# Kernel optimization log

Hardware: AMD Instinct MI355X
Metric: run time of the kernel (lower is better)

## Reference

```python
import jax, jax.numpy as jnp
import numpy as np

HK, WK = 7, 11  # local_k


def _local_mask(H, W):
    # Equivalent to the torch buffer: 0 inside the hk x wk window centered on the
    # query position (for odd hk, wk), -inf outside. Shape (N, N), N = H*W.
    n = jnp.arange(H * W)
    hq, wq = n // W, n % W
    dh = jnp.abs(hq[:, None] - hq[None, :])
    dw = jnp.abs(wq[:, None] - wq[None, :])
    allowed = (dh <= HK // 2) & (dw <= WK // 2)
    return jnp.where(allowed, 0.0, -jnp.inf).astype(jnp.float32)


def setup_inputs() -> dict:
    key = jax.random.key(0)
    k1, k2, k3 = jax.random.split(key, 3)
    B, H, W, C = 8, 32, 64, 512
    N = H * W
    x = jax.random.normal(k1, (B, N, C), dtype=jnp.float32)
    qkv_w = jax.random.normal(k2, (3 * C, C), dtype=jnp.float32) * (C ** -0.5)
    proj_w = jax.random.normal(k3, (C, C), dtype=jnp.float32) * (C ** -0.5)
    proj_b = jnp.zeros((C,), dtype=jnp.float32)
    return {"x": x, "qkv_w": qkv_w, "proj_w": proj_w, "proj_b": proj_b, "H": H, "W": W}


def reference(x, qkv_w, proj_w, proj_b, H, W):
    B, N, C = x.shape
    num_heads = 8
    head_dim = C // num_heads
    scale = head_dim ** -0.5

    # qkv: Linear(dim, 3*dim, bias=False) -> (B, N, 3, heads, head_dim)
    qkv = (x @ qkv_w.T).reshape(B, N, 3, num_heads, head_dim)
    q = qkv[:, :, 0].transpose(0, 2, 1, 3) * scale  # (B, h, N, d)
    k = qkv[:, :, 1].transpose(0, 2, 1, 3)
    v = qkv[:, :, 2].transpose(0, 2, 1, 3)

    attn = jnp.einsum('bhnd,bhmd->bhnm', q, k)  # (B, h, N, N)
    attn = attn + _local_mask(H, W)  # broadcast over (B, h)
    attn = jax.nn.softmax(attn, axis=-1)

    out = jnp.einsum('bhnm,bhmd->bhnd', attn, v)  # (B, h, N, d)
    out = out.transpose(0, 2, 1, 3).reshape(B, N, C)
    return out @ proj_w.T + proj_b
```

## Files before the change

### kernel.cpp

```cpp
#include <hip/hip_runtime.h>
#include <hip/hip_bf16.h>

#define B_SZ 8
#define H_SZ 32
#define W_SZ 64
#define N_SZ 2048
#define C_SZ 512
#define NH 8
#define HD 64

using u16 = unsigned short;
typedef __attribute__((ext_vector_type(8))) short s16x8;
typedef __attribute__((ext_vector_type(4))) float f32x4;

__device__ __forceinline__ float bf2f(u16 u) {
    union { unsigned int i; float f; } c; c.i = ((unsigned int)u) << 16; return c.f;
}
__device__ __forceinline__ u16 f2bf(float f) {
    union { float f; unsigned int i; } c; c.f = f;
    unsigned int r = c.i + 0x7fffu + ((c.i >> 16) & 1u);
    return (u16)(r >> 16);
}

#define GLL16(gp, lp) __builtin_amdgcn_global_load_lds( \
    (const __attribute__((address_space(1))) unsigned int*)(gp), \
    (__attribute__((address_space(3))) unsigned int*)(lp), 16, 0, 0)

__device__ __forceinline__ int lds_off(int row, int chunk) {
    return (row * 8 + (chunk ^ (row & 7))) * 8;
}

#define NX4 2097152
#define NQ4 196608
#define NP4 65536
__global__ __launch_bounds__(256)
void conv_all(const float* __restrict__ x, const float* __restrict__ qw,
              const float* __restrict__ pw, u16* __restrict__ xb,
              u16* __restrict__ qwb, u16* __restrict__ pwb)
{
    const int i = blockIdx.x * 256 + threadIdx.x;
    const float* src; u16* dst; int idx; float sc = 1.0f;
    if (i < NX4)             { src = x;  dst = xb;  idx = i; }
    else if (i < NX4 + NQ4)  { src = qw; dst = qwb; idx = i - NX4;
                               if (idx < 65536) sc = 0.125f; }
    else                     { src = pw; dst = pwb; idx = i - NX4 - NQ4; }
    const float4 v = ((const float4*)src)[idx];
    ushort4 o = { f2bf(v.x * sc), f2bf(v.y * sc), f2bf(v.z * sc), f2bf(v.w * sc) };
    ((ushort4*)dst)[idx] = o;
}

template<int MODE, int NB>
__global__ __launch_bounds__(512)
void gemm9(const u16* __restrict__ A, const u16* __restrict__ Bw,
           const float* __restrict__ bias,
           u16* __restrict__ q_ws, u16* __restrict__ k_ws, u16* __restrict__ v_ws,
           float* __restrict__ outp)
{
    __shared__ u16 As[3][256 * 64];
    __shared__ u16 Bs[3][128 * 64];
    const int t = threadIdx.x;
    const int chunk = gridDim.x >> 3;
    const int wg = (blockIdx.x & 7) * chunk + (blockIdx.x >> 3);
    const int m0 = (wg / NB) * 256;
    const int n0 = (wg % NB) * 128;
    const int wave = t >> 6, lane = t & 63;
    const int wm = (wave >> 2) * 128;
    const int wn = (wave & 3) * 32;
    const int l16 = lane & 15, quad = lane >> 4;
    const int srow = t >> 3;
    const int sch  = (t & 7) ^ (srow & 7);

    const u16* Ab = A  + (size_t)(m0 + srow) * C_SZ + sch * 8;
    const u16* Bb = Bw + (size_t)(n0 + srow) * C_SZ + sch * 8;

    f32x4 acc[8][2] = {};

#define SA(b, k0, g) GLL16(Ab + (size_t)(64 * (g)) * C_SZ + (k0), \
                           &As[b][(g) * 4096 + t * 8])
#define SB(b, k0, g) GLL16(Bb + (size_t)(64 * (g)) * C_SZ + (k0), \
                           &Bs[b][(g) * 4096 + t * 8])

    #pragma unroll
    for (int tb = 0; tb < 2; ++tb) {
        SA(tb, tb * 64, 0); SA(tb, tb * 64, 1); SA(tb, tb * 64, 2); SA(tb, tb * 64, 3);
        SB(tb, tb * 64, 0); SB(tb, tb * 64, 1);
    }
    asm volatile("s_waitcnt vmcnt(6)" ::: "memory");
    __builtin_amdgcn_s_barrier();
    __builtin_amdgcn_sched_barrier(0);

    #pragma unroll
    for (int tt = 0; tt < 8; ++tt) {
        const int ct = tt % 3;
        const int nt = (tt + 2) % 3;
        const int k2 = (tt + 2) * 64;

        s16x8 af[4][2], bf[2][2];
        #pragma unroll
        for (int i = 0; i < 4; ++i) {
            const int R = wm + 16 * i + l16;
            af[i][0] = *(const s16x8*)&As[ct][lds_off(R, quad)];
            af[i][1] = *(const s16x8*)&As[ct][lds_off(R, 4 + quad)];
        }
        #pragma unroll
        for (int j = 0; j < 2; ++j) {
            const int R = wn + 16 * j + l16;
            bf[j][0] = *(const s16x8*)&Bs[ct][lds_off(R, quad)];
            bf[j][1] = *(const s16x8*)&Bs[ct][lds_off(R, 4 + quad)];
        }
        if (tt < 6) { SA(nt, k2, 0); SA(nt, k2, 1); SB(nt, k2, 0); }
        __builtin_amdgcn_sched_barrier(0);
        __builtin_amdgcn_s_barrier();
        asm volatile("s_waitcnt lgkmcnt(0)" ::: "memory");
        __builtin_amdgcn_sched_barrier(0);
        __builtin_amdgcn_s_setprio(1);
        #pragma unroll
        for (int i = 0; i < 4; ++i)
            #pragma unroll
            for (int j = 0; j < 2; ++j) {
                acc[i][j] = __builtin_amdgcn_mfma_f32_16x16x32_bf16(af[i][0], bf[j][0], acc[i][j], 0, 0, 0);
                acc[i][j] = __builtin_amdgcn_mfma_f32_16x16x32_bf16(af[i][1], bf[j][1], acc[i][j], 0, 0, 0);
            }
        __builtin_amdgcn_s_setprio(0);
        __builtin_amdgcn_sched_barrier(0);
        __builtin_amdgcn_s_barrier();
        __builtin_amdgcn_sched_barrier(0);

        #pragma unroll
        for (int i = 0; i < 4; ++i) {
            const int R = wm + 64 + 16 * i + l16;
            af[i][0] = *(const s16x8*)&As[ct][lds_off(R, quad)];
            af[i][1] = *(const s16x8*)&As[ct][lds_off(R, 4 + quad)];
        }
        if (tt < 6) { SA(nt, k2, 2); SA(nt, k2, 3); SB(nt, k2, 1); }
        if (tt < 6)       asm volatile("s_waitcnt vmcnt(6)" ::: "memory");
        else if (tt == 6) asm volatile("s_waitcnt vmcnt(0)" ::: "memory");
        __builtin_amdgcn_sched_barrier(0);
        __builtin_amdgcn_s_barrier();
        asm volatile("s_waitcnt lgkmcnt(0)" ::: "memory");
        __builtin_amdgcn_sched_barrier(0);
        __builtin_amdgcn_s_setprio(1);
        #pragma unroll
        for (int i = 0; i < 4; ++i)
            #pragma unroll
            for (int j = 0; j < 2; ++j) {
                acc[4 + i][j] = __builtin_amdgcn_mfma_f32_16x16x32_bf16(af[i][0], bf[j][0], acc[4 + i][j], 0, 0, 0);
                acc[4 + i][j] = __builtin_amdgcn_mfma_f32_16x16x32_bf16(af[i][1], bf[j][1], acc[4 + i][j], 0, 0, 0);
            }
        __builtin_amdgcn_s_setprio(0);
        __builtin_amdgcn_sched_barrier(0);
        __builtin_amdgcn_s_barrier();
        __builtin_amdgcn_sched_barrier(0);
    }
#undef SA
#undef SB

    if (MODE == 0) {
        const int bb  = m0 >> 11;
        const int nnb = (m0 & 2047) + wm + (quad << 2);
        if (n0 >= 1024) {
            #pragma unroll
            for (int j = 0; j < 2; ++j) {
                const int c  = n0 - 1024 + wn + 16 * j + l16;
                const int h  = c >> 6, dd = c & 63;
                u16* vp = v_ws + (((size_t)bb * NH + h) * HD + dd) * N_SZ + nnb;
                #pragma unroll
                for (int i = 0; i < 8; ++i) {
                    ushort4 st = { f2bf(acc[i][j][0]), f2bf(acc[i][j][1]),
                                   f2bf(acc[i][j][2]), f2bf(acc[i][j][3]) };
                    *(ushort4*)(vp + 16 * i) = st;
                }
            }
        } else {
            u16* T = (n0 < 512) ? q_ws : k_ws;
            const int nq = n0 & 511;
            #pragma unroll
            for (int j = 0; j < 2; ++j) {
                const int gn = nq + wn + 16 * j + l16;
                const int h  = (gn >> 6) & 7, dd = gn & 63;
                u16* tp = T + (((size_t)bb * NH + h) * N_SZ + nnb) * HD + dd;
                #pragma unroll
                for (int i = 0; i < 8; ++i)
                    #pragma unroll
                    for (int r = 0; r < 4; ++r)
                        tp[(size_t)(16 * i + r) * HD] = f2bf(acc[i][j][r]);
            }
        }
    } else {
        #pragma unroll
        for (int j = 0; j < 2; ++j) {
            const int gn = n0 + wn + 16 * j + l16;
            const float bv = bias[gn];
            #pragma unroll
            for (int i = 0; i < 8; ++i)
                #pragma unroll
                for (int r = 0; r < 4; ++r)
                    outp[(size_t)(m0 + wm + 16 * i + (quad << 2) + r) * C_SZ + gn]
                        = acc[i][j][r] + bv;
        }
    }
}

__global__ __launch_bounds__(256)
void attn_mfma(const u16* __restrict__ q_ws, const u16* __restrict__ k_ws,
               const u16* __restrict__ vt_ws, u16* __restrict__ o_ws)
{
    __shared__ u16 KV[2][64 * 64];
    __shared__ u16 Ps[4][16 * 40];

    const int t = threadIdx.x, wave = t >> 6, lane = t & 63;
    const int l16 = lane & 15, quad = lane >> 4;
    const int u  = blockIdx.x;
    const int p  = u & 15;
    const int bh = u >> 4;
    const int r0 = 2 * p, r1 = 2 * p + 1;
    const size_t base = (size_t)bh * (N_SZ * HD);
    const int srow = t >> 3;
    const int sch  = (t & 7) ^ (srow & 7);

    const u16* qg = q_ws + base + (size_t)r0 * (64 * HD);
    u16* Qst = &KV[0][0];
    #pragma unroll
    for (int g = 0; g < 4; ++g)
        GLL16(qg + (size_t)(srow + 32 * g) * 64 + sch * 8, Qst + g * 2048 + t * 8);
    __syncthreads();

    s16x8 aQ[2][2];
    #pragma unroll
    for (int s = 0; s < 2; ++s) {
        const int Rq = 64 * s + 16 * wave + l16;
        aQ[s][0] = *(const s16x8*)&Qst[lds_off(Rq, quad)];
        aQ[s][1] = *(const s16x8*)&Qst[lds_off(Rq, 4 + quad)];
    }

    const int kb = min(max(16 * wave - 8, 0), 32);

    f32x4 accO[2][4] = {};
    float lp[2][4] = {};

    const int hlo = (r0 - 3 < 0) ? 0 : r0 - 3;
    const int hhi = (r1 + 3 > H_SZ - 1) ? H_SZ - 1 : r1 + 3;

    for (int hh = hlo; hh <= hhi; ++hh) {
        __syncthreads();
        const u16* kg = k_ws + base + (size_t)hh * (64 * HD);
        GLL16(kg + (size_t)srow        * 64 + sch * 8, &KV[0][t * 8]);
        GLL16(kg + (size_t)(srow + 32) * 64 + sch * 8, &KV[0][2048 + t * 8]);
        const u16* vg = vt_ws + base + (size_t)hh * 64;
        GLL16(vg + (size_t)srow        * N_SZ + sch * 8, &KV[1][t * 8]);
        GLL16(vg + (size_t)(srow + 32) * N_SZ + sch * 8, &KV[1][2048 + t * 8]);
        __syncthreads();

        s16x8 bK[2][2];
        #pragma unroll
        for (int j = 0; j < 2; ++j) {
            const int Rk = kb + 16 * j + l16;
            bK[j][0] = *(const s16x8*)&KV[0][lds_off(Rk, quad)];
            bK[j][1] = *(const s16x8*)&KV[0][lds_off(Rk, 4 + quad)];
        }
        s16x8 vf[4];
        #pragma unroll
        for (int j = 0; j < 4; ++j)
            vf[j] = *(const s16x8*)&KV[1][lds_off(16 * j + l16, (kb >> 3) + quad)];

        #pragma unroll
        for (int s = 0; s < 2; ++s) {
            const int dh = hh - (r0 + s);
            if (dh * dh > 9) continue;
            f32x4 z[2] = {{0.f,0.f,0.f,0.f},{0.f,0.f,0.f,0.f}};
            #pragma unroll
            for (int j = 0; j < 2; ++j) {
                z[j] = __builtin_amdgcn_mfma_f32_16x16x32_bf16(aQ[s][0], bK[j][0], z[j], 0, 0, 0);
                z[j] = __builtin_amdgcn_mfma_f32_16x16x32_bf16(aQ[s][1], bK[j][1], z[j], 0, 0, 0);
            }
            #pragma unroll
            for (int j = 0; j < 2; ++j) {
                const int ww = kb + 16 * j + l16;
                #pragma unroll
                for (int r = 0; r < 4; ++r) {
                    const int dw = ww - (16 * wave + quad * 4 + r);
                    const float pv = (dw * dw <= 25) ? __expf(z[j][r]) : 0.f;
                    const u16 pb = f2bf(pv);
                    lp[s][r] += bf2f(pb);
                    Ps[wave][(quad * 4 + r) * 40 + 16 * j + l16] = pb;
                }
            }
            s16x8 aP = *(const s16x8*)&Ps[wave][l16 * 40 + quad * 8];
            #pragma unroll
            for (int j = 0; j < 4; ++j)
                accO[s][j] = __builtin_amdgcn_mfma_f32_16x16x32_bf16(aP, vf[j], accO[s][j], 0, 0, 0);
        }
    }

    #pragma unroll
    for (int s = 0; s < 2; ++s)
        #pragma unroll
        for (int r = 0; r < 4; ++r) {
            lp[s][r] += __shfl_xor(lp[s][r], 1);
            lp[s][r] += __shfl_xor(lp[s][r], 2);
            lp[s][r] += __shfl_xor(lp[s][r], 4);
            lp[s][r] += __shfl_xor(lp[s][r], 8);
        }

    const int bb = bh >> 3, h = bh & 7;
    #pragma unroll
    for (int s = 0; s < 2; ++s)
        #pragma unroll
        for (int j = 0; j < 4; ++j)
            #pragma unroll
            for (int r = 0; r < 4; ++r) {
                const int row = (r0 + s) * 64 + 16 * wave + quad * 4 + r;
                o_ws[((size_t)bb * N_SZ + row) * C_SZ + h * 64 + 16 * j + l16]
                    = f2bf(accO[s][j][r] / lp[s][r]);
            }
}

extern "C" void kernel_launch(void* const* d_in, const int* in_sizes, int n_in,
                              void* d_out, int out_size, void* d_ws, size_t ws_size,
                              hipStream_t stream)
{
    const float* x      = (const float*)d_in[0];
    const float* qkv_w  = (const float*)d_in[1];
    const float* proj_w = (const float*)d_in[2];
    const float* proj_b = (const float*)d_in[3];
    float* outp = (float*)d_out;

    const size_t seg = (size_t)B_SZ * NH * N_SZ * HD;
    u16* q_ws = (u16*)d_ws;
    u16* k_ws = q_ws + seg;
    u16* v_ws = k_ws + seg;
    u16* o_ws = v_ws + seg;
    u16* xb   = o_ws + seg;
    u16* qwb  = xb + (size_t)16384 * 512;
    u16* pwb  = qwb + (size_t)1536 * 512;

    conv_all<<<9216, 256, 0, stream>>>(x, qkv_w, proj_w, xb, qwb, pwb);

    gemm9<0, 12><<<768, 512, 0, stream>>>(xb, qwb, nullptr,
                                          q_ws, k_ws, v_ws, nullptr);
    attn_mfma<<<B_SZ * NH * (H_SZ / 2), 256, 0, stream>>>(q_ws, k_ws, v_ws, o_ws);
    gemm9<1, 4><<<256, 512, 0, stream>>>(o_ws, pwb, proj_b,
                                         nullptr, nullptr, nullptr, outp);
}
```

Measured before the change: 177.0 us.

## Enlarge GEMM tile to 256x256 with double-buffered LDS pipeline

Widens each GEMM workgroup's N tile from 128 to 256, so each wave computes a 128x64 block. The LDS pipeline goes from three buffers to two, and the A and B loads for the next k-step are split across the four MFMA phases. This raises arithmetic intensity per LDS byte loaded and halves the grid size (384 and 128 blocks). The cost is more accumulator registers, possibly lower occupancy, and fewer blocks than the mi355x's 256 CUs for the projection GEMM, which may leave CUs idle.

```diff
diff --git a/kernel.cpp b/kernel.cpp
--- a/kernel.cpp
+++ b/kernel.cpp
@@ -51,21 +51,21 @@
 
 template<int MODE, int NB>
 __global__ __launch_bounds__(512)
-void gemm9(const u16* __restrict__ A, const u16* __restrict__ Bw,
-           const float* __restrict__ bias,
-           u16* __restrict__ q_ws, u16* __restrict__ k_ws, u16* __restrict__ v_ws,
-           float* __restrict__ outp)
+void gemm10(const u16* __restrict__ A, const u16* __restrict__ Bw,
+            const float* __restrict__ bias,
+            u16* __restrict__ q_ws, u16* __restrict__ k_ws, u16* __restrict__ v_ws,
+            float* __restrict__ outp)
 {
-    __shared__ u16 As[3][256 * 64];
-    __shared__ u16 Bs[3][128 * 64];
+    __shared__ u16 As[2][256 * 64];
+    __shared__ u16 Bs[2][256 * 64];
     const int t = threadIdx.x;
     const int chunk = gridDim.x >> 3;
     const int wg = (blockIdx.x & 7) * chunk + (blockIdx.x >> 3);
     const int m0 = (wg / NB) * 256;
-    const int n0 = (wg % NB) * 128;
+    const int n0 = (wg % NB) * 256;
     const int wave = t >> 6, lane = t & 63;
     const int wm = (wave >> 2) * 128;
-    const int wn = (wave & 3) * 32;
+    const int wn = (wave & 3) * 64;
     const int l16 = lane & 15, quad = lane >> 4;
     const int srow = t >> 3;
     const int sch  = (t & 7) ^ (srow & 7);
@@ -73,42 +73,40 @@
     const u16* Ab = A  + (size_t)(m0 + srow) * C_SZ + sch * 8;
     const u16* Bb = Bw + (size_t)(n0 + srow) * C_SZ + sch * 8;
 
-    f32x4 acc[8][2] = {};
-
-#define SA(b, k0, g) GLL16(Ab + (size_t)(64 * (g)) * C_SZ + (k0), \
-                           &As[b][(g) * 4096 + t * 8])
-#define SB(b, k0, g) GLL16(Bb + (size_t)(64 * (g)) * C_SZ + (k0), \
-                           &Bs[b][(g) * 4096 + t * 8])
-
-    #pragma unroll
-    for (int tb = 0; tb < 2; ++tb) {
-        SA(tb, tb * 64, 0); SA(tb, tb * 64, 1); SA(tb, tb * 64, 2); SA(tb, tb * 64, 3);
-        SB(tb, tb * 64, 0); SB(tb, tb * 64, 1);
-    }
-    asm volatile("s_waitcnt vmcnt(6)" ::: "memory");
+    f32x4 acc[8][4] = {};
+
+#define SA10(b, k0, g) GLL16(Ab + (size_t)(64 * (g)) * C_SZ + (k0), \
+                             &As[b][(g) * 4096 + t * 8])
+#define SB10(b, k0, g) GLL16(Bb + (size_t)(64 * (g)) * C_SZ + (k0), \
+                             &Bs[b][(g) * 4096 + t * 8])
+
+    SA10(0, 0, 0); SA10(0, 0, 1); SA10(0, 0, 2); SA10(0, 0, 3);
+    SB10(0, 0, 0); SB10(0, 0, 1); SB10(0, 0, 2); SB10(0, 0, 3);
+    asm volatile("s_waitcnt vmcnt(0)" ::: "memory");
     __builtin_amdgcn_s_barrier();
     __builtin_amdgcn_sched_barrier(0);
 
     #pragma unroll
     for (int tt = 0; tt < 8; ++tt) {
-        const int ct = tt % 3;
-        const int nt = (tt + 2) % 3;
-        const int k2 = (tt + 2) * 64;
-
-        s16x8 af[4][2], bf[2][2];
+        const int c  = tt & 1;
+        const int k1 = (tt + 1) * 64;
+        s16x8 af[4][2], bf[4][2];
+
         #pragma unroll
         for (int i = 0; i < 4; ++i) {
             const int R = wm + 16 * i + l16;
-            af[i][0] = *(const s16x8*)&As[ct][lds_off(R, quad)];
-            af[i][1] = *(const s16x8*)&As[ct][lds_off(R, 4 + quad)];
+            af[i][0] = *(const s16x8*)&As[c][lds_off(R, quad)];
+            af[i][1] = *(const s16x8*)&As[c][lds_off(R, 4 + quad)];
         }
         #pragma unroll
         for (int j = 0; j < 2; ++j) {
             const int R = wn + 16 * j + l16;
-            bf[j][0] = *(const s16x8*)&Bs[ct][lds_off(R, quad)];
-            bf[j][1] = *(const s16x8*)&Bs[ct][lds_off(R, 4 + quad)];
-        }
-        if (tt < 6) { SA(nt, k2, 0); SA(nt, k2, 1); SB(nt, k2, 0); }
+            bf[j][0] = *(const s16x8*)&Bs[c][lds_off(R, quad)];
+            bf[j][1] = *(const s16x8*)&Bs[c][lds_off(R, 4 + quad)];
+        }
+        if (tt < 7) { SA10(c ^ 1, k1, 0); SA10(c ^ 1, k1, 1);
+                      SA10(c ^ 1, k1, 2); SA10(c ^ 1, k1, 3); }
+        asm volatile("s_waitcnt lgkmcnt(8)" ::: "memory");
         __builtin_amdgcn_sched_barrier(0);
         __builtin_amdgcn_s_barrier();
         asm volatile("s_waitcnt lgkmcnt(0)" ::: "memory");
@@ -124,20 +122,56 @@
         __builtin_amdgcn_s_setprio(0);
         __builtin_amdgcn_sched_barrier(0);
         __builtin_amdgcn_s_barrier();
-        __builtin_amdgcn_sched_barrier(0);
+
+        #pragma unroll
+        for (int j = 2; j < 4; ++j) {
+            const int R = wn + 16 * j + l16;
+            bf[j][0] = *(const s16x8*)&Bs[c][lds_off(R, quad)];
+            bf[j][1] = *(const s16x8*)&Bs[c][lds_off(R, 4 + quad)];
+        }
+        if (tt < 7) { SB10(c ^ 1, k1, 0); SB10(c ^ 1, k1, 1);
+                      SB10(c ^ 1, k1, 2); SB10(c ^ 1, k1, 3); }
+        __builtin_amdgcn_sched_barrier(0);
+        __builtin_amdgcn_s_barrier();
+        asm volatile("s_waitcnt lgkmcnt(0)" ::: "memory");
+        __builtin_amdgcn_sched_barrier(0);
+        __builtin_amdgcn_s_setprio(1);
+        #pragma unroll
+        for (int i = 0; i < 4; ++i)
+            #pragma unroll
+            for (int j = 2; j < 4; ++j) {
+                acc[i][j] = __builtin_amdgcn_mfma_f32_16x16x32_bf16(af[i][0], bf[j][0], acc[i][j], 0, 0, 0);
+                acc[i][j] = __builtin_amdgcn_mfma_f32_16x16x32_bf16(af[i][1], bf[j][1], acc[i][j], 0, 0, 0);
+            }
+        __builtin_amdgcn_s_setprio(0);
+        __builtin_amdgcn_sched_barrier(0);
+        __builtin_amdgcn_s_barrier();
 
         #pragma unroll
         for (int i = 0; i < 4; ++i) {
             const int R = wm + 64 + 16 * i + l16;
-            af[i][0] = *(const s16x8*)&As[ct][lds_off(R, quad)];
-            af[i][1] = *(const s16x8*)&As[ct][lds_off(R, 4 + quad)];
-        }
-        if (tt < 6) { SA(nt, k2, 2); SA(nt, k2, 3); SB(nt, k2, 1); }
-        if (tt < 6)       asm volatile("s_waitcnt vmcnt(6)" ::: "memory");
-        else if (tt == 6) asm volatile("s_waitcnt vmcnt(0)" ::: "memory");
+            af[i][0] = *(const s16x8*)&As[c][lds_off(R, quad)];
+            af[i][1] = *(const s16x8*)&As[c][lds_off(R, 4 + quad)];
+        }
         __builtin_amdgcn_sched_barrier(0);
         __builtin_amdgcn_s_barrier();
         asm volatile("s_waitcnt lgkmcnt(0)" ::: "memory");
+        __builtin_amdgcn_sched_barrier(0);
+        __builtin_amdgcn_s_setprio(1);
+        #pragma unroll
+        for (int i = 0; i < 4; ++i)
+            #pragma unroll
+            for (int j = 2; j < 4; ++j) {
+                acc[4 + i][j] = __builtin_amdgcn_mfma_f32_16x16x32_bf16(af[i][0], bf[j][0], acc[4 + i][j], 0, 0, 0);
+                acc[4 + i][j] = __builtin_amdgcn_mfma_f32_16x16x32_bf16(af[i][1], bf[j][1], acc[4 + i][j], 0, 0, 0);
+            }
+        __builtin_amdgcn_s_setprio(0);
+        __builtin_amdgcn_sched_barrier(0);
+        __builtin_amdgcn_s_barrier();
+
+        if (tt < 7) asm volatile("s_waitcnt vmcnt(0)" ::: "memory");
+        __builtin_amdgcn_sched_barrier(0);
+        __builtin_amdgcn_s_barrier();
         __builtin_amdgcn_sched_barrier(0);
         __builtin_amdgcn_s_setprio(1);
         #pragma unroll
@@ -150,19 +184,18 @@
         __builtin_amdgcn_s_setprio(0);
         __builtin_amdgcn_sched_barrier(0);
         __builtin_amdgcn_s_barrier();
-        __builtin_amdgcn_sched_barrier(0);
     }
-#undef SA
-#undef SB
+#undef SA10
+#undef SB10
 
     if (MODE == 0) {
         const int bb  = m0 >> 11;
         const int nnb = (m0 & 2047) + wm + (quad << 2);
         if (n0 >= 1024) {
             #pragma unroll
-            for (int j = 0; j < 2; ++j) {
-                const int c  = n0 - 1024 + wn + 16 * j + l16;
-                const int h  = c >> 6, dd = c & 63;
+            for (int j = 0; j < 4; ++j) {
+                const int cc = n0 - 1024 + wn + 16 * j + l16;
+                const int h  = cc >> 6, dd = cc & 63;
                 u16* vp = v_ws + (((size_t)bb * NH + h) * HD + dd) * N_SZ + nnb;
                 #pragma unroll
                 for (int i = 0; i < 8; ++i) {
@@ -175,7 +208,7 @@
             u16* T = (n0 < 512) ? q_ws : k_ws;
             const int nq = n0 & 511;
             #pragma unroll
-            for (int j = 0; j < 2; ++j) {
+            for (int j = 0; j < 4; ++j) {
                 const int gn = nq + wn + 16 * j + l16;
                 const int h  = (gn >> 6) & 7, dd = gn & 63;
                 u16* tp = T + (((size_t)bb * NH + h) * N_SZ + nnb) * HD + dd;
@@ -188,7 +221,7 @@
         }
     } else {
         #pragma unroll
-        for (int j = 0; j < 2; ++j) {
+        for (int j = 0; j < 4; ++j) {
             const int gn = n0 + wn + 16 * j + l16;
             const float bv = bias[gn];
             #pragma unroll
@@ -336,9 +369,9 @@
 
     conv_all<<<9216, 256, 0, stream>>>(x, qkv_w, proj_w, xb, qwb, pwb);
 
-    gemm9<0, 12><<<768, 512, 0, stream>>>(xb, qwb, nullptr,
+    gemm10<0, 6><<<384, 512, 0, stream>>>(xb, qwb, nullptr,
                                           q_ws, k_ws, v_ws, nullptr);
     attn_mfma<<<B_SZ * NH * (H_SZ / 2), 256, 0, stream>>>(q_ws, k_ws, v_ws, o_ws);
-    gemm9<1, 4><<<256, 512, 0, stream>>>(o_ws, pwb, proj_b,
-                                         nullptr, nullptr, nullptr, outp);
-}
+    gemm10<1, 2><<<128, 512, 0, stream>>>(o_ws, pwb, proj_b,
+                                          nullptr, nullptr, nullptr, outp);
+}
```

Measured after the change: 185.9 us. 1.05x slower.
